# Optimization experiments

Hardware: AMD Instinct MI355X
Metric: run time of the kernel (lower is better)

## Reference

```python
import jax, jax.numpy as jnp
import numpy as np

EPS = 1e-12  # matches torch F.normalize default eps (clamp_min)
B, C, N = 32, 512, 4096
K_CLUSTERS, G_CLUSTERS = 64, 8
T_CLUSTERS = K_CLUSTERS + G_CLUSTERS  # 72
H_ATTN = T_CLUSTERS // 4  # 18


def _l2norm(v, axis):
    return v / jnp.maximum(jnp.linalg.norm(v, axis=axis, keepdims=True), EPS)


def setup_inputs() -> dict:
    key = jax.random.key(0)
    ks = jax.random.split(key, 6)
    x = jax.random.normal(ks[0], (B, C, N), dtype=jnp.float32)
    centroids = jax.random.normal(ks[1], (T_CLUSTERS, C), dtype=jnp.float32) * 0.01
    # 1x1 Conv2d(C -> T) == dense [T, C] weight + bias
    conv_w = jax.random.normal(ks[2], (T_CLUSTERS, C), dtype=jnp.float32) / np.sqrt(C).astype(np.float32)
    conv_b = jnp.zeros((T_CLUSTERS,), dtype=jnp.float32)
    ghost_weights = jnp.ones((G_CLUSTERS,), dtype=jnp.float32) * 0.1
    w1 = jax.random.normal(ks[3], (H_ATTN, T_CLUSTERS), dtype=jnp.float32) / np.sqrt(T_CLUSTERS).astype(np.float32)
    b1 = jnp.zeros((H_ATTN,), dtype=jnp.float32)
    w2 = jax.random.normal(ks[4], (T_CLUSTERS, H_ATTN), dtype=jnp.float32) / np.sqrt(H_ATTN).astype(np.float32)
    b2 = jnp.zeros((T_CLUSTERS,), dtype=jnp.float32)
    return {"x": x, "centroids": centroids, "conv_w": conv_w, "conv_b": conv_b,
            "ghost_weights": ghost_weights, "w1": w1, "b1": b1, "w2": w2, "b2": b2}


def reference(x, centroids, conv_w, conv_b, ghost_weights, w1, b1, w2, b2):
    # x: [B, C, N] -> L2 normalize over channel dim
    xn = _l2norm(x, axis=1)
    # 1x1 conv -> soft assignment logits [B, T, N], softmax over clusters
    logits = jnp.einsum('kc,bcn->bkn', conv_w, xn) + conv_b[None, :, None]
    assign = jax.nn.softmax(logits, axis=1)
    # residual aggregation, algebraically fused:
    # vlad[b,k,c] = sum_n a[b,k,n]*x[b,c,n] - centroid[k,c]*sum_n a[b,k,n]
    agg = jnp.einsum('bkn,bcn->bkc', assign, xn)
    mass = assign.sum(axis=-1)  # [B, T]
    vlad = agg - centroids[None, :, :] * mass[:, :, None]
    # ghost cluster down-weighting
    gw = jax.nn.softmax(ghost_weights)
    vlad = vlad.at[:, K_CLUSTERS:, :].multiply(gw[None, :, None])
    # attention over clusters: mean over C -> MLP -> softmax over clusters
    scores = vlad.mean(axis=-1)  # [B, T]
    h = jax.nn.relu(scores @ w1.T + b1)
    attn = jax.nn.softmax(h @ w2.T + b2, axis=1)
    vlad = vlad * attn[:, :, None]
    # intra-cluster L2 norm, drop ghosts, flatten, global L2 norm
    vlad = _l2norm(vlad, axis=2)
    vlad = vlad[:, :K_CLUSTERS, :].reshape(vlad.shape[0], -1)
    return _l2norm(vlad, axis=1)
```

## Files before the change

kernel.cpp:

```cpp
#include <hip/hip_runtime.h>
#include <hip/hip_bf16.h>

#define B_ 32
#define C_ 512
#define N_ 4096
#define T_ 72
#define K_ 64
#define KP 80
#define EPSF 1e-12f

typedef unsigned short u16;
typedef unsigned int u32;
typedef __attribute__((ext_vector_type(8))) short bf16x8;
typedef __attribute__((ext_vector_type(4))) float f32x4;

__device__ __forceinline__ u16 f2bf(float v) {
    __hip_bfloat16 h = __float2bfloat16(v);
    return *reinterpret_cast<u16*>(&h);
}

__global__ __launch_bounds__(256) void k_prep(
    const float* __restrict__ conv_w, const float* __restrict__ conv_b,
    u16* __restrict__ Wp, float* __restrict__ bp)
{
    const int idx = blockIdx.x * 256 + threadIdx.x;
    if (idx < KP * C_) {
        const int k = idx >> 9, c = idx & (C_ - 1);
        Wp[idx] = f2bf(k < T_ ? conv_w[k * C_ + c] : 0.f);
    } else if (idx < KP * C_ + KP) {
        const int j = idx - KP * C_;
        bp[j] = (j < T_) ? conv_b[j] : -1e30f;
    }
}

#define AN 64
__global__ __launch_bounds__(256) void k_assign(
    const float* __restrict__ x, const u16* __restrict__ Wp,
    const float* __restrict__ bp, u16* __restrict__ assignp,
    float* __restrict__ mass)
{
    __shared__ u16 xw[4][16][136];

    const int t  = threadIdx.x;
    const int b  = blockIdx.y;
    const int n0 = blockIdx.x * AN;

    const int lane = t & 63, w = t >> 6;
    const int q  = lane >> 4, nl = lane & 15;
    const int nq = lane & 3,  cg = lane >> 2;

    const float* xb = x + (size_t)b * C_ * N_ + n0 + 16 * w + 4 * nq;

    f32x4 acc[5];
    #pragma unroll
    for (int mt = 0; mt < 5; ++mt) acc[mt] = (f32x4)0.f;
    float ss[4] = {0.f, 0.f, 0.f, 0.f};

    float4 va[4], vc[4];
    #pragma unroll
    for (int ci = 0; ci < 4; ++ci) {
        const size_t coff = (size_t)(32 * ci + 2 * cg) * N_;
        va[ci] = *(const float4*)(xb + coff);
        vc[ci] = *(const float4*)(xb + coff + N_);
    }

    #pragma unroll
    for (int qtr = 0; qtr < 4; ++qtr) {
        #pragma unroll
        for (int ci = 0; ci < 4; ++ci) {
            const int cl = 32 * ci + 2 * cg;
            const float4 v0 = va[ci], v1 = vc[ci];
            ss[0] = fmaf(v0.x, v0.x, ss[0]); ss[0] = fmaf(v1.x, v1.x, ss[0]);
            ss[1] = fmaf(v0.y, v0.y, ss[1]); ss[1] = fmaf(v1.y, v1.y, ss[1]);
            ss[2] = fmaf(v0.z, v0.z, ss[2]); ss[2] = fmaf(v1.z, v1.z, ss[2]);
            ss[3] = fmaf(v0.w, v0.w, ss[3]); ss[3] = fmaf(v1.w, v1.w, ss[3]);
            *(u32*)&xw[w][4 * nq + 0][cl] = (u32)f2bf(v0.x) | ((u32)f2bf(v1.x) << 16);
            *(u32*)&xw[w][4 * nq + 1][cl] = (u32)f2bf(v0.y) | ((u32)f2bf(v1.y) << 16);
            *(u32*)&xw[w][4 * nq + 2][cl] = (u32)f2bf(v0.z) | ((u32)f2bf(v1.z) << 16);
            *(u32*)&xw[w][4 * nq + 3][cl] = (u32)f2bf(v0.w) | ((u32)f2bf(v1.w) << 16);
        }
        if (qtr < 3) {
            #pragma unroll
            for (int ci = 0; ci < 4; ++ci) {
                const size_t coff = (size_t)((qtr + 1) * 128 + 32 * ci + 2 * cg) * N_;
                va[ci] = *(const float4*)(xb + coff);
                vc[ci] = *(const float4*)(xb + coff + N_);
            }
        }
        const u16* wq = Wp + (size_t)nl * C_ + qtr * 128 + q * 8;
        #pragma unroll
        for (int ks = 0; ks < 4; ++ks) {
            const bf16x8 bfr = *(const bf16x8*)&xw[w][nl][ks * 32 + q * 8];
            #pragma unroll
            for (int mt = 0; mt < 5; ++mt) {
                const bf16x8 af = *(const bf16x8*)(wq + (size_t)(mt * 16) * C_ + ks * 32);
                acc[mt] = __builtin_amdgcn_mfma_f32_16x16x32_bf16(af, bfr, acc[mt], 0, 0, 0);
            }
        }
    }

    #pragma unroll
    for (int j = 0; j < 4; ++j) {
        ss[j] += __shfl_xor(ss[j], 4, 64);
        ss[j] += __shfl_xor(ss[j], 8, 64);
        ss[j] += __shfl_xor(ss[j], 16, 64);
        ss[j] += __shfl_xor(ss[j], 32, 64);
    }
    float inv[4];
    #pragma unroll
    for (int j = 0; j < 4; ++j) inv[j] = 1.0f / fmaxf(sqrtf(ss[j]), EPSF);

    const int src = nl >> 2;
    const float i0 = __shfl(inv[0], src, 64);
    const float i1 = __shfl(inv[1], src, 64);
    const float i2 = __shfl(inv[2], src, 64);
    const float i3 = __shfl(inv[3], src, 64);
    const float invn = (nl & 2) ? ((nl & 1) ? i3 : i2) : ((nl & 1) ? i1 : i0);
    const int nglob = n0 + 16 * w + nl;

    float lg[5][4];
    #pragma unroll
    for (int mt = 0; mt < 5; ++mt)
        #pragma unroll
        for (int r = 0; r < 4; ++r)
            lg[mt][r] = acc[mt][r] * invn + bp[mt * 16 + q * 4 + r];

    float mx = -1e30f;
    #pragma unroll
    for (int mt = 0; mt < 5; ++mt)
        #pragma unroll
        for (int r = 0; r < 4; ++r) mx = fmaxf(mx, lg[mt][r]);
    mx = fmaxf(mx, __shfl_xor(mx, 16, 64));
    mx = fmaxf(mx, __shfl_xor(mx, 32, 64));

    float s = 0.f;
    #pragma unroll
    for (int mt = 0; mt < 5; ++mt)
        #pragma unroll
        for (int r = 0; r < 4; ++r) {
            lg[mt][r] = __expf(lg[mt][r] - mx);
            s += lg[mt][r];
        }
    s += __shfl_xor(s, 16, 64);
    s += __shfl_xor(s, 32, 64);
    const float rs = 1.0f / s;

    #pragma unroll
    for (int mt = 0; mt < 4; ++mt)
        #pragma unroll
        for (int r = 0; r < 4; ++r) {
            const float a = lg[mt][r] * rs;
            float msum = a;
            msum += __shfl_xor(msum, 1, 64);
            msum += __shfl_xor(msum, 2, 64);
            msum += __shfl_xor(msum, 4, 64);
            msum += __shfl_xor(msum, 8, 64);
            const int k = mt * 16 + q * 4 + r;
            if (nl == 0) atomicAdd(&mass[b * K_ + k], msum);
            assignp[((size_t)b * K_ + k) * N_ + nglob] = f2bf(a * invn);
        }
}

#define GBK 64
#define NCH 8
__global__ __launch_bounds__(256) void k_agg(
    const float* __restrict__ x, const u16* __restrict__ assignp,
    float* __restrict__ out)
{
    __shared__ u16 Bt[4][16][72];

    const int t  = threadIdx.x;
    const int b  = blockIdx.z;
    const int nc0 = blockIdx.y * (N_ / NCH);
    const int c0  = blockIdx.x * 64;

    const int lane = t & 63, w = t >> 6;
    const int q = lane >> 4, nl = lane & 15;
    const int nq16 = lane & 15, cj = lane >> 4;

    f32x4 acc[4];
    #pragma unroll
    for (int mt = 0; mt < 4; ++mt) acc[mt] = (f32x4)0.f;

    const u16*   ab = assignp + (size_t)b * K_ * N_ + (size_t)nl * N_ + q * 8;
    const float* xb = x + ((size_t)b * C_ + c0 + 16 * w) * N_ + 4 * nq16;

    float4 vb[4];
    #pragma unroll
    for (int p = 0; p < 4; ++p)
        vb[p] = *(const float4*)(xb + (size_t)(4 * p + cj) * N_ + nc0);

    #pragma unroll 1
    for (int n0 = nc0; n0 < nc0 + N_ / NCH; n0 += GBK) {
        #pragma unroll
        for (int p = 0; p < 4; ++p) {
            const float4 v = vb[p];
            uint2 pk;
            pk.x = (u32)f2bf(v.x) | ((u32)f2bf(v.y) << 16);
            pk.y = (u32)f2bf(v.z) | ((u32)f2bf(v.w) << 16);
            *(uint2*)&Bt[w][4 * p + cj][4 * nq16] = pk;
        }
        if (n0 + GBK < nc0 + N_ / NCH) {
            #pragma unroll
            for (int p = 0; p < 4; ++p)
                vb[p] = *(const float4*)(xb + (size_t)(4 * p + cj) * N_ + n0 + GBK);
        }
        #pragma unroll
        for (int kk = 0; kk < 2; ++kk) {
            const bf16x8 bfr = *(const bf16x8*)&Bt[w][nl][kk * 32 + q * 8];
            #pragma unroll
            for (int mt = 0; mt < 4; ++mt) {
                const bf16x8 af = *(const bf16x8*)(ab + (size_t)(mt * 16) * N_ + n0 + kk * 32);
                acc[mt] = __builtin_amdgcn_mfma_f32_16x16x32_bf16(af, bfr, acc[mt], 0, 0, 0);
            }
        }
    }

    float* ob = out + (size_t)b * K_ * C_;
    const int c = c0 + 16 * w + nl;
    #pragma unroll
    for (int mt = 0; mt < 4; ++mt)
        #pragma unroll
        for (int r = 0; r < 4; ++r)
            atomicAdd(&ob[(size_t)(mt * 16 + q * 4 + r) * C_ + c], acc[mt][r]);
}

__device__ __forceinline__ float block_reduce_sum_256(float v) {
    #pragma unroll
    for (int o = 32; o > 0; o >>= 1) v += __shfl_down(v, o, 64);
    __shared__ float wsh[4];
    const int lane = threadIdx.x & 63, wid = threadIdx.x >> 6;
    if (lane == 0) wsh[wid] = v;
    __syncthreads();
    float r = 0.f;
    if (threadIdx.x == 0) r = wsh[0] + wsh[1] + wsh[2] + wsh[3];
    return r;
}

__global__ __launch_bounds__(256) void k_rnorm(
    const float* __restrict__ agg, const float* __restrict__ centroids,
    const float* __restrict__ mass, float* __restrict__ rnorm,
    float* __restrict__ gsum)
{
    const int k = blockIdx.x, b = blockIdx.y;
    const float mk = mass[b * K_ + k];
    const float* p  = agg + ((size_t)b * K_ + k) * C_;
    const float* cb = centroids + k * C_;
    float s = 0.f;
    #pragma unroll 2
    for (int i = threadIdx.x; i < C_; i += 256) {
        const float v = fmaf(-cb[i], mk, p[i]);
        s = fmaf(v, v, s);
    }
    const float ss = block_reduce_sum_256(s);
    if (threadIdx.x == 0) {
        const float rn = fmaxf(sqrtf(ss), EPSF);
        rnorm[b * K_ + k] = rn;
        atomicAdd(gsum + b, ss / (rn * rn));
    }
}

__global__ __launch_bounds__(256) void k_final(
    float* __restrict__ out, const float* __restrict__ centroids,
    const float* __restrict__ mass, const float* __restrict__ rnorm,
    const float* __restrict__ gsum)
{
    const size_t i4 = ((size_t)blockIdx.x * 256 + threadIdx.x) * 4;
    const int b = (int)(i4 >> 15);
    const int k = (int)((i4 >> 9) & 63);
    const int c = (int)(i4 & 511);
    const float gn = fmaxf(sqrtf(gsum[b]), EPSF);
    const float sc = 1.0f / (rnorm[b * K_ + k] * gn);
    const float mk = mass[b * K_ + k];
    float4 v  = *(const float4*)(out + i4);
    const float4 cv = *(const float4*)(centroids + k * C_ + c);
    v.x = fmaf(-cv.x, mk, v.x) * sc;
    v.y = fmaf(-cv.y, mk, v.y) * sc;
    v.z = fmaf(-cv.z, mk, v.z) * sc;
    v.w = fmaf(-cv.w, mk, v.w) * sc;
    *(float4*)(out + i4) = v;
}

extern "C" void kernel_launch(void* const* d_in, const int* in_sizes, int n_in,
                              void* d_out, int out_size, void* d_ws, size_t ws_size,
                              hipStream_t stream) {
    const float* x         = (const float*)d_in[0];
    const float* centroids = (const float*)d_in[1];
    const float* conv_w    = (const float*)d_in[2];
    const float* conv_b    = (const float*)d_in[3];

    float* out = (float*)d_out;
    char*  ws  = (char*)d_ws;

    u16*   assignp = (u16*)ws;
    u16*   Wp      = (u16*)(ws + 16777216);
    float* bpad    = (float*)(ws + 16777216 + 81920);
    float* mass    = (float*)(ws + 16777216 + 81920 + 320);
    float* rnorm   = mass + B_ * K_;
    float* gsum    = rnorm + B_ * K_;

    hipMemsetAsync(mass, 0, B_ * K_ * sizeof(float), stream);
    hipMemsetAsync(gsum, 0, B_ * sizeof(float), stream);
    hipMemsetAsync(out, 0, (size_t)out_size * sizeof(float), stream);

    k_prep<<<dim3((KP * C_ + KP + 255) / 256), 256, 0, stream>>>(conv_w, conv_b, Wp, bpad);
    k_assign<<<dim3(N_ / AN, B_), 256, 0, stream>>>(x, Wp, bpad, assignp, mass);
    k_agg<<<dim3(C_ / 64, NCH, B_), 256, 0, stream>>>(x, assignp, out);
    k_rnorm<<<dim3(K_, B_), 256, 0, stream>>>(out, centroids, mass, rnorm, gsum);
    k_final<<<(out_size / 4 + 255) / 256, 256, 0, stream>>>(out, centroids, mass, rnorm, gsum);
}
```

Before: 571.6 us.

## Restructure assign kernel to 256-column tiles with shared W fragment reuse

The assignment GEMM kernel now has each block handle 256 spatial positions instead of 64. All four waves cooperatively stage 32-channel chunks of x into a swizzled shared buffer. Each wave computes four 16-column tiles, reusing W fragments held in registers across them, and W loads are software-prefetched one chunk ahead. This cuts redundant global W loads and raises MFMA work per load, at the cost of more accumulator registers, block-wide barriers each chunk, and a 4x smaller grid (512 blocks).

```diff
diff --git a/kernel.cpp b/kernel.cpp
--- a/kernel.cpp
+++ b/kernel.cpp
@@ -33,132 +33,148 @@
     }
 }
 
-#define AN 64
-__global__ __launch_bounds__(256) void k_assign(
+#define ANW 256
+__global__ __launch_bounds__(256, 2) void k_assign(
     const float* __restrict__ x, const u16* __restrict__ Wp,
     const float* __restrict__ bp, u16* __restrict__ assignp,
     float* __restrict__ mass)
 {
-    __shared__ u16 xw[4][16][136];
-
-    const int t  = threadIdx.x;
-    const int b  = blockIdx.y;
-    const int n0 = blockIdx.x * AN;
-
+    __shared__ u16   xs[ANW * 32];
+    __shared__ float red[4][ANW];
+    __shared__ float inv_sh[ANW];
+
+    const int t = threadIdx.x;
+    const int b = blockIdx.y;
+    const int n0 = blockIdx.x * ANW;
     const int lane = t & 63, w = t >> 6;
-    const int q  = lane >> 4, nl = lane & 15;
-    const int nq = lane & 3,  cg = lane >> 2;
-
-    const float* xb = x + (size_t)b * C_ * N_ + n0 + 16 * w + 4 * nq;
-
-    f32x4 acc[5];
-    #pragma unroll
-    for (int mt = 0; mt < 5; ++mt) acc[mt] = (f32x4)0.f;
+    const int q = lane >> 4, nl = lane & 15;
+
+    const float* xb = x + (size_t)b * C_ * N_ + n0 + 4 * lane;
+
+    f32x4 acc[4][5];
+    #pragma unroll
+    for (int nt = 0; nt < 4; ++nt)
+        #pragma unroll
+        for (int mt = 0; mt < 5; ++mt) acc[nt][mt] = (f32x4)0.f;
     float ss[4] = {0.f, 0.f, 0.f, 0.f};
 
-    float4 va[4], vc[4];
-    #pragma unroll
-    for (int ci = 0; ci < 4; ++ci) {
-        const size_t coff = (size_t)(32 * ci + 2 * cg) * N_;
-        va[ci] = *(const float4*)(xb + coff);
-        vc[ci] = *(const float4*)(xb + coff + N_);
-    }
-
-    #pragma unroll
-    for (int qtr = 0; qtr < 4; ++qtr) {
-        #pragma unroll
-        for (int ci = 0; ci < 4; ++ci) {
-            const int cl = 32 * ci + 2 * cg;
-            const float4 v0 = va[ci], v1 = vc[ci];
-            ss[0] = fmaf(v0.x, v0.x, ss[0]); ss[0] = fmaf(v1.x, v1.x, ss[0]);
-            ss[1] = fmaf(v0.y, v0.y, ss[1]); ss[1] = fmaf(v1.y, v1.y, ss[1]);
-            ss[2] = fmaf(v0.z, v0.z, ss[2]); ss[2] = fmaf(v1.z, v1.z, ss[2]);
-            ss[3] = fmaf(v0.w, v0.w, ss[3]); ss[3] = fmaf(v1.w, v1.w, ss[3]);
-            *(u32*)&xw[w][4 * nq + 0][cl] = (u32)f2bf(v0.x) | ((u32)f2bf(v1.x) << 16);
-            *(u32*)&xw[w][4 * nq + 1][cl] = (u32)f2bf(v0.y) | ((u32)f2bf(v1.y) << 16);
-            *(u32*)&xw[w][4 * nq + 2][cl] = (u32)f2bf(v0.z) | ((u32)f2bf(v1.z) << 16);
-            *(u32*)&xw[w][4 * nq + 3][cl] = (u32)f2bf(v0.w) | ((u32)f2bf(v1.w) << 16);
-        }
-        if (qtr < 3) {
-            #pragma unroll
-            for (int ci = 0; ci < 4; ++ci) {
-                const size_t coff = (size_t)((qtr + 1) * 128 + 32 * ci + 2 * cg) * N_;
-                va[ci] = *(const float4*)(xb + coff);
-                vc[ci] = *(const float4*)(xb + coff + N_);
+    float4 v[8];
+    bf16x8 af[5];
+    #pragma unroll
+    for (int i = 0; i < 8; ++i)
+        v[i] = *(const float4*)(xb + (size_t)(w * 8 + i) * N_);
+    #pragma unroll
+    for (int mt = 0; mt < 5; ++mt)
+        af[mt] = *(const bf16x8*)(Wp + (size_t)(mt * 16 + nl) * C_ + q * 8);
+
+#define VJ(i) (j == 0 ? v[i].x : j == 1 ? v[i].y : j == 2 ? v[i].z : v[i].w)
+
+    #pragma unroll 1
+    for (int ch = 0; ch < 16; ++ch) {
+        #pragma unroll
+        for (int j = 0; j < 4; ++j) {
+            const float f0 = VJ(0), f1 = VJ(1), f2 = VJ(2), f3 = VJ(3);
+            const float f4 = VJ(4), f5 = VJ(5), f6 = VJ(6), f7 = VJ(7);
+            ss[j] = fmaf(f0, f0, ss[j]); ss[j] = fmaf(f1, f1, ss[j]);
+            ss[j] = fmaf(f2, f2, ss[j]); ss[j] = fmaf(f3, f3, ss[j]);
+            ss[j] = fmaf(f4, f4, ss[j]); ss[j] = fmaf(f5, f5, ss[j]);
+            ss[j] = fmaf(f6, f6, ss[j]); ss[j] = fmaf(f7, f7, ss[j]);
+            uint4 pk;
+            pk.x = (u32)f2bf(f0) | ((u32)f2bf(f1) << 16);
+            pk.y = (u32)f2bf(f2) | ((u32)f2bf(f3) << 16);
+            pk.z = (u32)f2bf(f4) | ((u32)f2bf(f5) << 16);
+            pk.w = (u32)f2bf(f6) | ((u32)f2bf(f7) << 16);
+            const int n = 4 * lane + j;
+            const int slot = (w + ((lane >> 1) & 3)) & 3;
+            *(uint4*)&xs[n * 32 + slot * 8] = pk;
+        }
+        __syncthreads();
+        if (ch < 15) {
+            #pragma unroll
+            for (int i = 0; i < 8; ++i)
+                v[i] = *(const float4*)(xb + (size_t)((ch + 1) * 32 + w * 8 + i) * N_);
+        }
+        __builtin_amdgcn_sched_barrier(0);
+        #pragma unroll
+        for (int nt = 0; nt < 4; ++nt) {
+            const int n = (4 * w + nt) * 16 + nl;
+            const int slot = (q + ((n >> 3) & 3)) & 3;
+            const bf16x8 bfr = *(const bf16x8*)&xs[n * 32 + slot * 8];
+            #pragma unroll
+            for (int mt = 0; mt < 5; ++mt)
+                acc[nt][mt] = __builtin_amdgcn_mfma_f32_16x16x32_bf16(af[mt], bfr, acc[nt][mt], 0, 0, 0);
+        }
+        if (ch < 15) {
+            #pragma unroll
+            for (int mt = 0; mt < 5; ++mt)
+                af[mt] = *(const bf16x8*)(Wp + (size_t)(mt * 16 + nl) * C_ + (ch + 1) * 32 + q * 8);
+        }
+        __syncthreads();
+    }
+#undef VJ
+
+    *(float4*)&red[w][4 * lane] = make_float4(ss[0], ss[1], ss[2], ss[3]);
+    __syncthreads();
+    {
+        const float s = red[0][t] + red[1][t] + red[2][t] + red[3][t];
+        inv_sh[t] = 1.0f / fmaxf(sqrtf(s), EPSF);
+    }
+    __syncthreads();
+
+    float bpv[5][4];
+    #pragma unroll
+    for (int mt = 0; mt < 5; ++mt)
+        #pragma unroll
+        for (int r = 0; r < 4; ++r) bpv[mt][r] = bp[mt * 16 + q * 4 + r];
+
+    #pragma unroll
+    for (int nt = 0; nt < 4; ++nt) {
+        const int n_loc = (4 * w + nt) * 16 + nl;
+        const float invn = inv_sh[n_loc];
+        const int nglob = n0 + n_loc;
+
+        float lg[5][4];
+        #pragma unroll
+        for (int mt = 0; mt < 5; ++mt)
+            #pragma unroll
+            for (int r = 0; r < 4; ++r)
+                lg[mt][r] = acc[nt][mt][r] * invn + bpv[mt][r];
+
+        float mx = -1e30f;
+        #pragma unroll
+        for (int mt = 0; mt < 5; ++mt)
+            #pragma unroll
+            for (int r = 0; r < 4; ++r) mx = fmaxf(mx, lg[mt][r]);
+        mx = fmaxf(mx, __shfl_xor(mx, 16, 64));
+        mx = fmaxf(mx, __shfl_xor(mx, 32, 64));
+
+        float s = 0.f;
+        #pragma unroll
+        for (int mt = 0; mt < 5; ++mt)
+            #pragma unroll
+            for (int r = 0; r < 4; ++r) {
+                lg[mt][r] = __expf(lg[mt][r] - mx);
+                s += lg[mt][r];
             }
-        }
-        const u16* wq = Wp + (size_t)nl * C_ + qtr * 128 + q * 8;
-        #pragma unroll
-        for (int ks = 0; ks < 4; ++ks) {
-            const bf16x8 bfr = *(const bf16x8*)&xw[w][nl][ks * 32 + q * 8];
-            #pragma unroll
-            for (int mt = 0; mt < 5; ++mt) {
-                const bf16x8 af = *(const bf16x8*)(wq + (size_t)(mt * 16) * C_ + ks * 32);
-                acc[mt] = __builtin_amdgcn_mfma_f32_16x16x32_bf16(af, bfr, acc[mt], 0, 0, 0);
+        s += __shfl_xor(s, 16, 64);
+        s += __shfl_xor(s, 32, 64);
+        const float rs = 1.0f / s;
+
+        #pragma unroll
+        for (int mt = 0; mt < 4; ++mt)
+            #pragma unroll
+            for (int r = 0; r < 4; ++r) {
+                const float a = lg[mt][r] * rs;
+                float msum = a;
+                msum += __shfl_xor(msum, 1, 64);
+                msum += __shfl_xor(msum, 2, 64);
+                msum += __shfl_xor(msum, 4, 64);
+                msum += __shfl_xor(msum, 8, 64);
+                const int k = mt * 16 + q * 4 + r;
+                if (nl == 0) atomicAdd(&mass[b * K_ + k], msum);
+                assignp[((size_t)b * K_ + k) * N_ + nglob] = f2bf(a * invn);
             }
-        }
-    }
-
-    #pragma unroll
-    for (int j = 0; j < 4; ++j) {
-        ss[j] += __shfl_xor(ss[j], 4, 64);
-        ss[j] += __shfl_xor(ss[j], 8, 64);
-        ss[j] += __shfl_xor(ss[j], 16, 64);
-        ss[j] += __shfl_xor(ss[j], 32, 64);
-    }
-    float inv[4];
-    #pragma unroll
-    for (int j = 0; j < 4; ++j) inv[j] = 1.0f / fmaxf(sqrtf(ss[j]), EPSF);
-
-    const int src = nl >> 2;
-    const float i0 = __shfl(inv[0], src, 64);
-    const float i1 = __shfl(inv[1], src, 64);
-    const float i2 = __shfl(inv[2], src, 64);
-    const float i3 = __shfl(inv[3], src, 64);
-    const float invn = (nl & 2) ? ((nl & 1) ? i3 : i2) : ((nl & 1) ? i1 : i0);
-    const int nglob = n0 + 16 * w + nl;
-
-    float lg[5][4];
-    #pragma unroll
-    for (int mt = 0; mt < 5; ++mt)
-        #pragma unroll
-        for (int r = 0; r < 4; ++r)
-            lg[mt][r] = acc[mt][r] * invn + bp[mt * 16 + q * 4 + r];
-
-    float mx = -1e30f;
-    #pragma unroll
-    for (int mt = 0; mt < 5; ++mt)
-        #pragma unroll
-        for (int r = 0; r < 4; ++r) mx = fmaxf(mx, lg[mt][r]);
-    mx = fmaxf(mx, __shfl_xor(mx, 16, 64));
-    mx = fmaxf(mx, __shfl_xor(mx, 32, 64));
-
-    float s = 0.f;
-    #pragma unroll
-    for (int mt = 0; mt < 5; ++mt)
-        #pragma unroll
-        for (int r = 0; r < 4; ++r) {
-            lg[mt][r] = __expf(lg[mt][r] - mx);
-            s += lg[mt][r];
-        }
-    s += __shfl_xor(s, 16, 64);
-    s += __shfl_xor(s, 32, 64);
-    const float rs = 1.0f / s;
-
-    #pragma unroll
-    for (int mt = 0; mt < 4; ++mt)
-        #pragma unroll
-        for (int r = 0; r < 4; ++r) {
-            const float a = lg[mt][r] * rs;
-            float msum = a;
-            msum += __shfl_xor(msum, 1, 64);
-            msum += __shfl_xor(msum, 2, 64);
-            msum += __shfl_xor(msum, 4, 64);
-            msum += __shfl_xor(msum, 8, 64);
-            const int k = mt * 16 + q * 4 + r;
-            if (nl == 0) atomicAdd(&mass[b * K_ + k], msum);
-            assignp[((size_t)b * K_ + k) * N_ + nglob] = f2bf(a * invn);
-        }
+    }
 }
 
 #define GBK 64
@@ -304,7 +320,7 @@
     hipMemsetAsync(out, 0, (size_t)out_size * sizeof(float), stream);
 
     k_prep<<<dim3((KP * C_ + KP + 255) / 256), 256, 0, stream>>>(conv_w, conv_b, Wp, bpad);
-    k_assign<<<dim3(N_ / AN, B_), 256, 0, stream>>>(x, Wp, bpad, assignp, mass);
+    k_assign<<<dim3(N_ / ANW, B_), 256, 0, stream>>>(x, Wp, bpad, assignp, mass);
     k_agg<<<dim3(C_ / 64, NCH, B_), 256, 0, stream>>>(x, assignp, out);
     k_rnorm<<<dim3(K_, B_), 256, 0, stream>>>(out, centroids, mass, rnorm, gsum);
     k_final<<<(out_size / 4 + 255) / 256, 256, 0, stream>>>(out, centroids, mass, rnorm, gsum);
```

Result: faster. 507.6 us (-11.2%).
